# Kernel tuning notes

Measured on AMD Instinct MI355X. Metric: run time of the kernel, lower is better.

Reference implementation:

```python
import jax, jax.numpy as jnp
import numpy as np

T, B, I, L = 512, 64, 512, 1024

def setup_inputs() -> dict:
    key = jax.random.key(0)
    k1, k2, k3, k4 = jax.random.split(key, 4)
    s_i = 1.0 / np.sqrt(I)
    s_l = 1.0 / np.sqrt(L)
    x = jax.random.normal(k1, (T, B, I), dtype=jnp.float32)
    h = jnp.zeros((B, L), dtype=jnp.float32)
    Wi = jax.random.uniform(k2, (L, I), minval=-s_i, maxval=s_i, dtype=jnp.float32)
    bi = jax.random.uniform(k3, (L,), minval=-s_i, maxval=s_i, dtype=jnp.float32)
    Wh = jax.random.uniform(k4, (L, L), minval=-s_l, maxval=s_l, dtype=jnp.float32)
    return {"x": x, "h": h, "Wi": Wi, "bi": bi, "Wh": Wh}

def reference(x, h, Wi, bi, Wh):
    # Precompute input projection for all timesteps in one big GEMM: [T,B,L]
    xi = jnp.einsum('tbi,li->tbl', x, Wi) + bi

    def step(h, xi_t):
        h_new = jnp.tanh(xi_t + h @ Wh.T)  # [B,L]
        return h_new, h_new

    _, h_output = jax.lax.scan(step, h, xi)  # [T,B,L]
    return h_output
```

## Files before the change

### kernel.cpp

```cpp
#include <hip/hip_runtime.h>

#define TT 512
#define BB 64
#define II 512
#define LL 1024
#define GROUPS 16
#define RPG 4
#define WPG 16
#define NWGS (GROUPS * WPG)

typedef __bf16 bf16x8 __attribute__((ext_vector_type(8)));
typedef float f32x4 __attribute__((ext_vector_type(4)));
typedef unsigned int u32x4 __attribute__((ext_vector_type(4)));

#define WSWI_OFF 0u
#define WSWH_OFF (1u << 20)
#define HBUF_OFF (3u << 20)

__device__ __forceinline__ unsigned short f2bf(float f) {
  unsigned int u = __builtin_bit_cast(unsigned int, f);
  u += 0x7fffu + ((u >> 16) & 1u);
  return (unsigned short)(u >> 16);
}

__device__ __forceinline__ bf16x8 ld_frag(const unsigned short* p) {
  return __builtin_bit_cast(bf16x8, *(const uint4*)p);
}

__global__ __launch_bounds__(256) void prep_kernel(
    const float* __restrict__ h0, const float* __restrict__ Wi,
    const float* __restrict__ Wh, unsigned short* __restrict__ wsWi,
    unsigned short* __restrict__ wsWh2, unsigned short* __restrict__ hbuf) {
  int idx = blockIdx.x * 256 + threadIdx.x;
  const float* src;
  unsigned short* dst;
  bool tagme = false;
  if (idx < 65536) {
    int ln = idx & 63, s = idx >> 6;
    int nsub = s & 7, s2 = s >> 3, ks = s2 & 15, bn = s2 >> 4;
    int n = bn * 128 + nsub * 16 + (ln & 15);
    int k = ks * 32 + (ln >> 4) * 8;
    src = Wi + (size_t)n * II + k;
    dst = wsWi + (size_t)idx * 8;
  } else if (idx < 196608) {
    int o = idx - 65536;
    int l = o & 63, s = o >> 6;
    int ks = s & 31, s2 = s >> 5;
    int n4 = s2 & 3, w = s2 >> 2;
    int col = w * 64 + n4 * 16 + (l & 15);
    int k = ks * 32 + (l >> 4) * 8;
    src = Wh + (size_t)col * LL + k;
    dst = wsWh2 + (size_t)o * 8;
  } else if (idx < 204800) {
    int o = idx - 196608;
    int r = o & 3, kq = (o >> 2) & 3, ks = (o >> 4) & 31, g = o >> 9;
    src = h0 + (size_t)(g * RPG + r) * LL + ks * 32 + kq * 8;
    dst = hbuf + (size_t)o * 8;
    tagme = true;
  } else if (idx < 212992) {
    int o = idx - 204800;
    uint4 p = {0x00010001u, 0x00010001u, 0x00010001u, 0x00010001u};
    *(uint4*)(hbuf + 65536 + (size_t)o * 8) = p;
    return;
  } else {
    return;
  }
  float4 a0 = *(const float4*)src;
  float4 a1 = *(const float4*)(src + 4);
  uint4 p;
  p.x = f2bf(a0.x) | ((unsigned)f2bf(a0.y) << 16);
  p.y = f2bf(a0.z) | ((unsigned)f2bf(a0.w) << 16);
  p.z = f2bf(a1.x) | ((unsigned)f2bf(a1.y) << 16);
  p.w = f2bf(a1.z) | ((unsigned)f2bf(a1.w) << 16);
  if (tagme) {
    p.x &= ~1u; p.y &= ~1u; p.z &= ~1u; p.w &= ~1u;
  }
  *(uint4*)dst = p;
}

__global__ __launch_bounds__(256) void xi_gemm(
    const float* __restrict__ x, const float* __restrict__ bi,
    const unsigned short* __restrict__ wsWi, float* __restrict__ out) {
  __shared__ unsigned short As[8 * 64 * 8];
  __shared__ unsigned short Bs[8 * 64 * 8];
  const int tid = threadIdx.x;
  const int ln = tid & 63;
  const int wv = tid >> 6;
  const int wm = wv >> 1, wn = wv & 1;
  const int bn = blockIdx.x;
  const int Mbase = blockIdx.y * 128;
  const int Nbase = bn * 128;

  f32x4 acc[4][4] = {};

  for (int ks = 0; ks < 16; ++ks) {
    __syncthreads();
#pragma unroll
    for (int i = 0; i < 2; ++i) {
      int slot = tid + 256 * i;
      int msub = slot >> 6;
      int l2 = slot & 63;
      const float* src =
          x + (size_t)(Mbase + msub * 16 + (l2 & 15)) * II + ks * 32 + (l2 >> 4) * 8;
      float4 a0 = *(const float4*)src;
      float4 a1 = *(const float4*)(src + 4);
      uint4 p;
      p.x = f2bf(a0.x) | ((unsigned)f2bf(a0.y) << 16);
      p.y = f2bf(a0.z) | ((unsigned)f2bf(a0.w) << 16);
      p.z = f2bf(a1.x) | ((unsigned)f2bf(a1.y) << 16);
      p.w = f2bf(a1.z) | ((unsigned)f2bf(a1.w) << 16);
      *(uint4*)(As + slot * 8) = p;
      const uint4* bsrc = (const uint4*)(wsWi + (size_t)(bn * 16 + ks) * 4096) + slot;
      *(uint4*)(Bs + slot * 8) = *bsrc;
    }
    __syncthreads();
    bf16x8 af[4];
#pragma unroll
    for (int m = 0; m < 4; ++m)
      af[m] = ld_frag(As + ((wm * 4 + m) * 64 + ln) * 8);
#pragma unroll
    for (int n = 0; n < 4; ++n) {
      bf16x8 bf = ld_frag(Bs + ((wn * 4 + n) * 64 + ln) * 8);
#pragma unroll
      for (int m = 0; m < 4; ++m)
        acc[m][n] = __builtin_amdgcn_mfma_f32_16x16x32_bf16(af[m], bf, acc[m][n], 0, 0, 0);
    }
  }
#pragma unroll
  for (int n = 0; n < 4; ++n) {
    int col = Nbase + wn * 64 + n * 16 + (ln & 15);
    float bv = bi[col];
#pragma unroll
    for (int m = 0; m < 4; ++m) {
      int row0 = Mbase + wm * 64 + m * 16 + (ln >> 4) * 4;
#pragma unroll
      for (int r = 0; r < 4; ++r)
        out[(size_t)(row0 + r) * LL + col] = acc[m][n][r] + bv;
    }
  }
}

__global__ __launch_bounds__(256, 1) void scan_kernel(
    const unsigned short* __restrict__ wsWh2, float* __restrict__ out,
    unsigned short* __restrict__ hbuf) {
  __shared__ unsigned short hA[2][4096];
  __shared__ unsigned short packb[4][64];

  const int tid = threadIdx.x;
  const int ln = tid & 63;
  const int wv = tid >> 6;
  const int g = blockIdx.x >> 4;
  const int w = blockIdx.x & 15;
  const int kq = ln >> 4;
  const int rdup = ln & 3;
  const int cc = ln & 15;
  const int ks_w = w * 2 + (wv >> 1);
  const int half = wv & 1;

  u32x4 Breg[32];
  {
    const unsigned short* bsrc = wsWh2 + (size_t)(w * 4 + wv) * 16384 + ln * 8;
#pragma unroll
    for (int i = 0; i < 8; ++i) {
      const unsigned short* bp = bsrc + i * 2048;
      asm volatile(
          "global_load_dwordx4 %0, %4, off\n\t"
          "global_load_dwordx4 %1, %4, off offset:1024\n\t"
          "global_load_dwordx4 %2, %4, off offset:2048\n\t"
          "global_load_dwordx4 %3, %4, off offset:3072"
          : "=&v"(Breg[i * 4]), "=&v"(Breg[i * 4 + 1]),
            "=&v"(Breg[i * 4 + 2]), "=&v"(Breg[i * 4 + 3])
          : "v"(bp) : "memory");
    }
    asm volatile("s_waitcnt vmcnt(0)" ::: "memory");
    __builtin_amdgcn_sched_barrier(0);
  }

  const int c0 = tid, c1 = tid + 256;

  const size_t ocell = (size_t)(g * RPG + kq) * LL + w * 64 + wv * 16 + cc;

  float xv_next;
  asm volatile("global_load_dword %0, %1, off"
               : "=&v"(xv_next) : "v"(out + ocell) : "memory");

  for (int t = 0; t < TT; ++t) {
    const unsigned ptag = (unsigned)((t >> 1) & 1);
    const unsigned ntag = (unsigned)(((t + 1) >> 1) & 1);

    const unsigned short* hcur = hbuf + (size_t)(t & 1) * 65536 + g * 4096;
    const unsigned short* p0 = hcur + c0 * 8;
    const unsigned short* p1 = hcur + c1 * 8;
    u32x4 hv0, hv1;
    {
      int good;
      do {
        asm volatile(
            "global_load_dwordx4 %0, %2, off sc1\n\t"
            "global_load_dwordx4 %1, %3, off sc1\n\t"
            "s_waitcnt vmcnt(0)"
            : "=&v"(hv0), "=&v"(hv1) : "v"(p0), "v"(p1) : "memory");
        good = ((hv0[0] & 1) == ptag) & ((hv0[1] & 1) == ptag) &
               ((hv0[2] & 1) == ptag) & ((hv0[3] & 1) == ptag) &
               ((hv1[0] & 1) == ptag) & ((hv1[1] & 1) == ptag) &
               ((hv1[2] & 1) == ptag) & ((hv1[3] & 1) == ptag);
      } while (__all(good) == 0);
    }
    __builtin_amdgcn_sched_barrier(0);
    unsigned short* hw = hA[t & 1];
    *(u32x4*)(hw + c0 * 8) = hv0;
    *(u32x4*)(hw + c1 * 8) = hv1;
    float xv = xv_next;
    __syncthreads();

    f32x4 a0 = {}, a1 = {}, a2 = {}, a3 = {};
#pragma unroll
    for (int ks = 0; ks < 32; ks += 4) {
      bf16x8 A0 = ld_frag(hw + (ks * 16 + kq * 4 + rdup) * 8);
      bf16x8 A1 = ld_frag(hw + ((ks + 1) * 16 + kq * 4 + rdup) * 8);
      bf16x8 A2 = ld_frag(hw + ((ks + 2) * 16 + kq * 4 + rdup) * 8);
      bf16x8 A3 = ld_frag(hw + ((ks + 3) * 16 + kq * 4 + rdup) * 8);
      a0 = __builtin_amdgcn_mfma_f32_16x16x32_bf16(
          A0, __builtin_bit_cast(bf16x8, Breg[ks]), a0, 0, 0, 0);
      a1 = __builtin_amdgcn_mfma_f32_16x16x32_bf16(
          A1, __builtin_bit_cast(bf16x8, Breg[ks + 1]), a1, 0, 0, 0);
      a2 = __builtin_amdgcn_mfma_f32_16x16x32_bf16(
          A2, __builtin_bit_cast(bf16x8, Breg[ks + 2]), a2, 0, 0, 0);
      a3 = __builtin_amdgcn_mfma_f32_16x16x32_bf16(
          A3, __builtin_bit_cast(bf16x8, Breg[ks + 3]), a3, 0, 0, 0);
    }
    f32x4 s = (a0 + a1) + (a2 + a3);

    float hval = tanhf(s[kq] + xv);
    unsigned short hbf = f2bf(hval);
    if ((cc & 1) == 0)
      hbf = (unsigned short)((hbf & ~1u) | ntag);
    packb[wv][(cc >> 3) * 32 + kq * 8 + (cc & 7)] = hbf;
    asm volatile("s_waitcnt lgkmcnt(0)" ::: "memory");
    __builtin_amdgcn_sched_barrier(0);

    unsigned short* hnext = hbuf + (size_t)((t + 1) & 1) * 65536 + g * 4096;
    if (ln < 8) {
      u32x4 pk = *(const u32x4*)(&packb[wv][ln * 8]);
      unsigned short* dp = hnext + ks_w * 128 + half * 64 + ln * 8;
      asm volatile("global_store_dwordx4 %0, %1, off sc1"
                   :: "v"(dp), "v"(pk) : "memory");
    }
    out[(size_t)t * 65536 + ocell] = hval;
    {
      int tn = (t + 1 < TT) ? (t + 1) : t;
      asm volatile("global_load_dword %0, %1, off"
                   : "=&v"(xv_next) : "v"(out + (size_t)tn * 65536 + ocell)
                   : "memory");
    }
  }
}

extern "C" void kernel_launch(void* const* d_in, const int* in_sizes, int n_in,
                              void* d_out, int out_size, void* d_ws, size_t ws_size,
                              hipStream_t stream) {
  const float* x  = (const float*)d_in[0];
  const float* h0 = (const float*)d_in[1];
  const float* Wi = (const float*)d_in[2];
  const float* bi = (const float*)d_in[3];
  const float* Wh = (const float*)d_in[4];
  float* out = (float*)d_out;
  char* ws = (char*)d_ws;
  unsigned short* wsWi  = (unsigned short*)(ws + WSWI_OFF);
  unsigned short* wsWh2 = (unsigned short*)(ws + WSWH_OFF);
  unsigned short* hbuf  = (unsigned short*)(ws + HBUF_OFF);

  prep_kernel<<<832, 256, 0, stream>>>(h0, Wi, Wh, wsWi, wsWh2, hbuf);
  xi_gemm<<<dim3(8, 256), 256, 0, stream>>>(x, bi, wsWi, out);
  void* args[] = {(void*)&wsWh2, (void*)&out, (void*)&hbuf};
  (void)hipLaunchCooperativeKernel(reinterpret_cast<void*>(scan_kernel),
                                   dim3(NWGS), dim3(256), args, 0, stream);
}
```

Measured before the change: 1.064 ms.

## Interleave two batch groups per workgroup and prefetch hidden state via async LDS loads

Halves the scan grid to 128 workgroups, each handling two independent batch groups in alternation. While one group computes, the hidden state for the other is loaded straight into LDS with global_load_lds, which is meant to hide the cross-workgroup polling latency. The tag check now reads LDS and falls back to a spin loop on global memory only when data is stale. Each workgroup does twice the serial work per step, and the prefetch may pick up stale data that forces extra reloads.

```diff
diff --git a/kernel.cpp b/kernel.cpp
--- a/kernel.cpp
+++ b/kernel.cpp
@@ -6,8 +6,7 @@
 #define LL 1024
 #define GROUPS 16
 #define RPG 4
-#define WPG 16
-#define NWGS (GROUPS * WPG)
+#define NWGS 128
 
 typedef __bf16 bf16x8 __attribute__((ext_vector_type(8)));
 typedef float f32x4 __attribute__((ext_vector_type(4)));
@@ -16,6 +15,11 @@
 #define WSWI_OFF 0u
 #define WSWH_OFF (1u << 20)
 #define HBUF_OFF (3u << 20)
+
+#define GLDS16(gp_, lp_)                                                    \
+  __builtin_amdgcn_global_load_lds(                                         \
+      (const __attribute__((address_space(1))) void*)(const void*)(gp_),    \
+      (__attribute__((address_space(3))) void*)(void*)(lp_), 16, 0, 16)
 
 __device__ __forceinline__ unsigned short f2bf(float f) {
   unsigned int u = __builtin_bit_cast(unsigned int, f);
@@ -25,6 +29,12 @@
 
 __device__ __forceinline__ bf16x8 ld_frag(const unsigned short* p) {
   return __builtin_bit_cast(bf16x8, *(const uint4*)p);
+}
+
+__device__ __forceinline__ int tagok(u32x4 a, u32x4 b, unsigned p) {
+  return (int)(((a[0] & 1) == p) & ((a[1] & 1) == p) & ((a[2] & 1) == p) &
+               ((a[3] & 1) == p) & ((b[0] & 1) == p) & ((b[1] & 1) == p) &
+               ((b[2] & 1) == p) & ((b[3] & 1) == p));
 }
 
 __global__ __launch_bounds__(256) void prep_kernel(
@@ -143,14 +153,15 @@
 __global__ __launch_bounds__(256, 1) void scan_kernel(
     const unsigned short* __restrict__ wsWh2, float* __restrict__ out,
     unsigned short* __restrict__ hbuf) {
-  __shared__ unsigned short hA[2][4096];
+  __shared__ unsigned short hA[2][2][4096];
   __shared__ unsigned short packb[4][64];
 
   const int tid = threadIdx.x;
   const int ln = tid & 63;
   const int wv = tid >> 6;
-  const int g = blockIdx.x >> 4;
+  const int gp = blockIdx.x >> 4;
   const int w = blockIdx.x & 15;
+  const int g0 = gp, g1 = gp + 8;
   const int kq = ln >> 4;
   const int rdup = ln & 3;
   const int cc = ln & 15;
@@ -176,81 +187,159 @@
     __builtin_amdgcn_sched_barrier(0);
   }
 
-  const int c0 = tid, c1 = tid + 256;
-
-  const size_t ocell = (size_t)(g * RPG + kq) * LL + w * 64 + wv * 16 + cc;
-
-  float xv_next;
+  const size_t ocell0 = (size_t)(g0 * RPG + kq) * LL + w * 64 + wv * 16 + cc;
+  const size_t ocell1 = (size_t)(g1 * RPG + kq) * LL + w * 64 + wv * 16 + cc;
+
+  GLDS16(hbuf + g0 * 4096 + tid * 8, &hA[0][0][wv * 512]);
+  GLDS16(hbuf + g0 * 4096 + (tid + 256) * 8, &hA[0][0][2048 + wv * 512]);
+  float xv0n, xv1n;
   asm volatile("global_load_dword %0, %1, off"
-               : "=&v"(xv_next) : "v"(out + ocell) : "memory");
+               : "=&v"(xv0n) : "v"(out + ocell0) : "memory");
+  asm volatile("global_load_dword %0, %1, off"
+               : "=&v"(xv1n) : "v"(out + ocell1) : "memory");
 
   for (int t = 0; t < TT; ++t) {
     const unsigned ptag = (unsigned)((t >> 1) & 1);
     const unsigned ntag = (unsigned)(((t + 1) >> 1) & 1);
 
-    const unsigned short* hcur = hbuf + (size_t)(t & 1) * 65536 + g * 4096;
-    const unsigned short* p0 = hcur + c0 * 8;
-    const unsigned short* p1 = hcur + c1 * 8;
-    u32x4 hv0, hv1;
     {
-      int good;
-      do {
-        asm volatile(
-            "global_load_dwordx4 %0, %2, off sc1\n\t"
-            "global_load_dwordx4 %1, %3, off sc1\n\t"
-            "s_waitcnt vmcnt(0)"
-            : "=&v"(hv0), "=&v"(hv1) : "v"(p0), "v"(p1) : "memory");
-        good = ((hv0[0] & 1) == ptag) & ((hv0[1] & 1) == ptag) &
-               ((hv0[2] & 1) == ptag) & ((hv0[3] & 1) == ptag) &
-               ((hv1[0] & 1) == ptag) & ((hv1[1] & 1) == ptag) &
-               ((hv1[2] & 1) == ptag) & ((hv1[3] & 1) == ptag);
-      } while (__all(good) == 0);
-    }
-    __builtin_amdgcn_sched_barrier(0);
-    unsigned short* hw = hA[t & 1];
-    *(u32x4*)(hw + c0 * 8) = hv0;
-    *(u32x4*)(hw + c1 * 8) = hv1;
-    float xv = xv_next;
-    __syncthreads();
-
-    f32x4 a0 = {}, a1 = {}, a2 = {}, a3 = {};
-#pragma unroll
-    for (int ks = 0; ks < 32; ks += 4) {
-      bf16x8 A0 = ld_frag(hw + (ks * 16 + kq * 4 + rdup) * 8);
-      bf16x8 A1 = ld_frag(hw + ((ks + 1) * 16 + kq * 4 + rdup) * 8);
-      bf16x8 A2 = ld_frag(hw + ((ks + 2) * 16 + kq * 4 + rdup) * 8);
-      bf16x8 A3 = ld_frag(hw + ((ks + 3) * 16 + kq * 4 + rdup) * 8);
-      a0 = __builtin_amdgcn_mfma_f32_16x16x32_bf16(
-          A0, __builtin_bit_cast(bf16x8, Breg[ks]), a0, 0, 0, 0);
-      a1 = __builtin_amdgcn_mfma_f32_16x16x32_bf16(
-          A1, __builtin_bit_cast(bf16x8, Breg[ks + 1]), a1, 0, 0, 0);
-      a2 = __builtin_amdgcn_mfma_f32_16x16x32_bf16(
-          A2, __builtin_bit_cast(bf16x8, Breg[ks + 2]), a2, 0, 0, 0);
-      a3 = __builtin_amdgcn_mfma_f32_16x16x32_bf16(
-          A3, __builtin_bit_cast(bf16x8, Breg[ks + 3]), a3, 0, 0, 0);
-    }
-    f32x4 s = (a0 + a1) + (a2 + a3);
-
-    float hval = tanhf(s[kq] + xv);
-    unsigned short hbf = f2bf(hval);
-    if ((cc & 1) == 0)
-      hbf = (unsigned short)((hbf & ~1u) | ntag);
-    packb[wv][(cc >> 3) * 32 + kq * 8 + (cc & 7)] = hbf;
-    asm volatile("s_waitcnt lgkmcnt(0)" ::: "memory");
-    __builtin_amdgcn_sched_barrier(0);
-
-    unsigned short* hnext = hbuf + (size_t)((t + 1) & 1) * 65536 + g * 4096;
-    if (ln < 8) {
-      u32x4 pk = *(const u32x4*)(&packb[wv][ln * 8]);
-      unsigned short* dp = hnext + ks_w * 128 + half * 64 + ln * 8;
-      asm volatile("global_store_dwordx4 %0, %1, off sc1"
-                   :: "v"(dp), "v"(pk) : "memory");
-    }
-    out[(size_t)t * 65536 + ocell] = hval;
-    {
+      unsigned short* hw = &hA[0][t & 1][0];
+      const unsigned short* hc = hbuf + (size_t)(t & 1) * 65536 + g0 * 4096;
+      if (t == 0) asm volatile("s_waitcnt vmcnt(0)" ::: "memory");
+      else        asm volatile("s_waitcnt vmcnt(3)" ::: "memory");
+      __builtin_amdgcn_sched_barrier(0);
+      u32x4 v0 = *(const u32x4*)(hw + tid * 8);
+      u32x4 v1 = *(const u32x4*)(hw + (tid + 256) * 8);
+      int good = tagok(v0, v1, ptag);
+      if (!good) {
+        do {
+          asm volatile(
+              "global_load_dwordx4 %0, %2, off sc1\n\t"
+              "global_load_dwordx4 %1, %3, off sc1\n\t"
+              "s_waitcnt vmcnt(0)"
+              : "=&v"(v0), "=&v"(v1)
+              : "v"(hc + tid * 8), "v"(hc + (tid + 256) * 8) : "memory");
+          good = tagok(v0, v1, ptag);
+        } while (!good);
+        *(u32x4*)(hw + tid * 8) = v0;
+        *(u32x4*)(hw + (tid + 256) * 8) = v1;
+      }
+      float xv = xv0n;
+      asm volatile("s_waitcnt lgkmcnt(0)" ::: "memory");
+      __builtin_amdgcn_s_barrier();
+      asm volatile("" ::: "memory");
+      __builtin_amdgcn_sched_barrier(0);
+
+      f32x4 a0 = {}, a1 = {}, a2 = {}, a3 = {};
+#pragma unroll
+      for (int ks = 0; ks < 32; ks += 4) {
+        bf16x8 A0 = ld_frag(hw + (ks * 16 + kq * 4 + rdup) * 8);
+        bf16x8 A1 = ld_frag(hw + ((ks + 1) * 16 + kq * 4 + rdup) * 8);
+        bf16x8 A2 = ld_frag(hw + ((ks + 2) * 16 + kq * 4 + rdup) * 8);
+        bf16x8 A3 = ld_frag(hw + ((ks + 3) * 16 + kq * 4 + rdup) * 8);
+        a0 = __builtin_amdgcn_mfma_f32_16x16x32_bf16(
+            A0, __builtin_bit_cast(bf16x8, Breg[ks]), a0, 0, 0, 0);
+        a1 = __builtin_amdgcn_mfma_f32_16x16x32_bf16(
+            A1, __builtin_bit_cast(bf16x8, Breg[ks + 1]), a1, 0, 0, 0);
+        a2 = __builtin_amdgcn_mfma_f32_16x16x32_bf16(
+            A2, __builtin_bit_cast(bf16x8, Breg[ks + 2]), a2, 0, 0, 0);
+        a3 = __builtin_amdgcn_mfma_f32_16x16x32_bf16(
+            A3, __builtin_bit_cast(bf16x8, Breg[ks + 3]), a3, 0, 0, 0);
+      }
+      f32x4 s = (a0 + a1) + (a2 + a3);
+
+      float hval = tanhf(s[kq] + xv);
+      unsigned short hbf = f2bf(hval);
+      if ((cc & 1) == 0) hbf = (unsigned short)((hbf & ~1u) | ntag);
+      packb[wv][(cc >> 3) * 32 + kq * 8 + (cc & 7)] = hbf;
+      asm volatile("s_waitcnt lgkmcnt(0)" ::: "memory");
+      __builtin_amdgcn_sched_barrier(0);
+
+      const unsigned short* pn = hbuf + (size_t)(t & 1) * 65536 + g1 * 4096;
+      GLDS16(pn + tid * 8, &hA[1][t & 1][wv * 512]);
+      GLDS16(pn + (tid + 256) * 8, &hA[1][t & 1][2048 + wv * 512]);
+
+      unsigned short* hn = hbuf + (size_t)((t + 1) & 1) * 65536 + g0 * 4096;
+      if (ln < 8) {
+        u32x4 pk = *(const u32x4*)(&packb[wv][ln * 8]);
+        asm volatile("global_store_dwordx4 %0, %1, off sc1"
+                     :: "v"(hn + ks_w * 128 + half * 64 + ln * 8), "v"(pk)
+                     : "memory");
+      }
+      out[(size_t)t * 65536 + ocell0] = hval;
       int tn = (t + 1 < TT) ? (t + 1) : t;
       asm volatile("global_load_dword %0, %1, off"
-                   : "=&v"(xv_next) : "v"(out + (size_t)tn * 65536 + ocell)
+                   : "=&v"(xv0n) : "v"(out + (size_t)tn * 65536 + ocell0)
+                   : "memory");
+    }
+
+    {
+      unsigned short* hw = &hA[1][t & 1][0];
+      const unsigned short* hc = hbuf + (size_t)(t & 1) * 65536 + g1 * 4096;
+      asm volatile("s_waitcnt vmcnt(3)" ::: "memory");
+      __builtin_amdgcn_sched_barrier(0);
+      u32x4 v0 = *(const u32x4*)(hw + tid * 8);
+      u32x4 v1 = *(const u32x4*)(hw + (tid + 256) * 8);
+      int good = tagok(v0, v1, ptag);
+      if (!good) {
+        do {
+          asm volatile(
+              "global_load_dwordx4 %0, %2, off sc1\n\t"
+              "global_load_dwordx4 %1, %3, off sc1\n\t"
+              "s_waitcnt vmcnt(0)"
+              : "=&v"(v0), "=&v"(v1)
+              : "v"(hc + tid * 8), "v"(hc + (tid + 256) * 8) : "memory");
+          good = tagok(v0, v1, ptag);
+        } while (!good);
+        *(u32x4*)(hw + tid * 8) = v0;
+        *(u32x4*)(hw + (tid + 256) * 8) = v1;
+      }
+      float xv = xv1n;
+      asm volatile("s_waitcnt lgkmcnt(0)" ::: "memory");
+      __builtin_amdgcn_s_barrier();
+      asm volatile("" ::: "memory");
+      __builtin_amdgcn_sched_barrier(0);
+
+      f32x4 a0 = {}, a1 = {}, a2 = {}, a3 = {};
+#pragma unroll
+      for (int ks = 0; ks < 32; ks += 4) {
+        bf16x8 A0 = ld_frag(hw + (ks * 16 + kq * 4 + rdup) * 8);
+        bf16x8 A1 = ld_frag(hw + ((ks + 1) * 16 + kq * 4 + rdup) * 8);
+        bf16x8 A2 = ld_frag(hw + ((ks + 2) * 16 + kq * 4 + rdup) * 8);
+        bf16x8 A3 = ld_frag(hw + ((ks + 3) * 16 + kq * 4 + rdup) * 8);
+        a0 = __builtin_amdgcn_mfma_f32_16x16x32_bf16(
+            A0, __builtin_bit_cast(bf16x8, Breg[ks]), a0, 0, 0, 0);
+        a1 = __builtin_amdgcn_mfma_f32_16x16x32_bf16(
+            A1, __builtin_bit_cast(bf16x8, Breg[ks + 1]), a1, 0, 0, 0);
+        a2 = __builtin_amdgcn_mfma_f32_16x16x32_bf16(
+            A2, __builtin_bit_cast(bf16x8, Breg[ks + 2]), a2, 0, 0, 0);
+        a3 = __builtin_amdgcn_mfma_f32_16x16x32_bf16(
+            A3, __builtin_bit_cast(bf16x8, Breg[ks + 3]), a3, 0, 0, 0);
+      }
+      f32x4 s = (a0 + a1) + (a2 + a3);
+
+      float hval = tanhf(s[kq] + xv);
+      unsigned short hbf = f2bf(hval);
+      if ((cc & 1) == 0) hbf = (unsigned short)((hbf & ~1u) | ntag);
+      packb[wv][(cc >> 3) * 32 + kq * 8 + (cc & 7)] = hbf;
+      asm volatile("s_waitcnt lgkmcnt(0)" ::: "memory");
+      __builtin_amdgcn_sched_barrier(0);
+
+      const unsigned short* pn = hbuf + (size_t)((t + 1) & 1) * 65536 + g0 * 4096;
+      GLDS16(pn + tid * 8, &hA[0][(t + 1) & 1][wv * 512]);
+      GLDS16(pn + (tid + 256) * 8, &hA[0][(t + 1) & 1][2048 + wv * 512]);
+
+      unsigned short* hn = hbuf + (size_t)((t + 1) & 1) * 65536 + g1 * 4096;
+      if (ln < 8) {
+        u32x4 pk = *(const u32x4*)(&packb[wv][ln * 8]);
+        asm volatile("global_store_dwordx4 %0, %1, off sc1"
+                     :: "v"(hn + ks_w * 128 + half * 64 + ln * 8), "v"(pk)
+                     : "memory");
+      }
+      out[(size_t)t * 65536 + ocell1] = hval;
+      int tn = (t + 1 < TT) ? (t + 1) : t;
+      asm volatile("global_load_dword %0, %1, off"
+                   : "=&v"(xv1n) : "v"(out + (size_t)tn * 65536 + ocell1)
                    : "memory");
     }
   }
```

After: 1.468 ms. +37.9%, slower.
